# Kernel tuning notes

Measured on AMD Instinct MI355X. Metric: run time of the kernel, lower is better.

The kernel has to match this reference:

```python
import jax, jax.numpy as jnp
import numpy as np

B, T, D, H = 2, 2048, 1024, 16
HD = D // H


def sinusoidal_rel_pe(seq_len, d_model, dtype=jnp.float32):
    # Relative positions T-1 .. 0 (reversed), standard sin/cos interleave.
    pos = jnp.arange(seq_len - 1, -1, -1, dtype=jnp.float32)[:, None]  # [T,1]
    div = jnp.exp(-jnp.log(jnp.float32(10000.0)) * jnp.arange(0, d_model, 2, dtype=jnp.float32) / d_model)
    pe = jnp.zeros((seq_len, d_model), dtype=jnp.float32)
    pe = pe.at[:, 0::2].set(jnp.sin(pos * div))
    pe = pe.at[:, 1::2].set(jnp.cos(pos * div))
    return pe.astype(dtype)


def relative_to_absolute(x):
    # x: [B,H,T,L] with L == T. Music-Transformer skew trick.
    b, h, t1, l = x.shape
    x = jnp.pad(x, ((0, 0), (0, 0), (0, 0), (1, 0)))          # pad left of last dim
    x = x.reshape(b, h, -1)
    x = jnp.pad(x, ((0, 0), (0, 0), (l - t1, 0)))
    x = x.reshape(b, h, 1 + t1, l)
    return x[:, :, 1:]


def setup_inputs() -> dict:
    key = jax.random.key(0)
    k1, k2, k3 = jax.random.split(key, 3)
    x = jax.random.normal(k1, (B, T, D), dtype=jnp.float32)
    # causal mask: True where attention is disallowed (j > i)
    mask = jnp.triu(jnp.ones((T, T), dtype=bool), k=1)[None, None]
    mask = jnp.broadcast_to(mask, (B, 1, T, T))
    Wqkv = jax.random.normal(k2, (D, 3 * D), dtype=jnp.float32) * 0.02
    Wout = jax.random.normal(k3, (D, D), dtype=jnp.float32) * 0.02
    bout = jnp.zeros((D,), dtype=jnp.float32)
    return {"x": x, "mask": mask, "Wqkv": Wqkv, "Wout": Wout, "bout": bout}


def reference(x, mask, Wqkv, Wout, bout):
    b, t, d = x.shape
    scale = jnp.sqrt(jnp.float32(HD)).astype(x.dtype)
    qkv = x @ Wqkv                                  # [B,T,3D]
    q, k, v = jnp.split(qkv, 3, axis=-1)
    E = sinusoidal_rel_pe(t, d, x.dtype)            # [T,D], constant rel bias
    q = q.reshape(b, t, H, HD).transpose(0, 2, 1, 3)   # [B,H,T,hd]
    k = k.reshape(b, t, H, HD).transpose(0, 2, 1, 3)
    v = v.reshape(b, t, H, HD).transpose(0, 2, 1, 3)
    Eh = E.reshape(t, H, HD).transpose(1, 0, 2)        # [H,T,hd]
    att_k = jnp.einsum('bhqd,bhkd->bhqk', q, k)
    att_e = relative_to_absolute(jnp.einsum('bhqd,hkd->bhqk', q, Eh))
    score = (att_k + att_e) / scale
    score = jnp.where(mask, -jnp.inf, score)
    score = jax.nn.softmax(score, axis=-1)          # dropout is identity (eval)
    ctx = jnp.einsum('bhqk,bhkd->bhqd', score, v)
    ctx = ctx.transpose(0, 2, 1, 3).reshape(b, t, d)
    out = ctx @ Wout + bout
    return (out, score)
```

## Files before the change

kernel.cpp:

```cpp
#include <hip/hip_runtime.h>

typedef __bf16 bf16x8 __attribute__((ext_vector_type(8)));
typedef float f32x4 __attribute__((ext_vector_type(4)));

#define B_ 2
#define T_ 2048
#define D_ 1024
#define H_ 16

__device__ __forceinline__ ushort f2bf(float f) {
  union { float f; unsigned u; } v; v.f = f;
  unsigned u = v.u;
  return (ushort)((u + 0x7FFFu + ((u >> 16) & 1u)) >> 16);
}

__device__ __forceinline__ void g2l16(const void* g, void* l) {
  __builtin_amdgcn_global_load_lds(
      (const __attribute__((address_space(1))) unsigned int*)g,
      (__attribute__((address_space(3))) unsigned int*)l, 16, 0, 0);
}

__global__ __launch_bounds__(256) void cvt_kernel(const float* __restrict__ in,
                                                  ushort* __restrict__ out) {
  int i = (blockIdx.x * 256 + threadIdx.x) * 4;
  float4 v = *(const float4*)(in + i);
  ushort4 o;
  o.x = f2bf(v.x); o.y = f2bf(v.y); o.z = f2bf(v.z); o.w = f2bf(v.w);
  *(ushort4*)(out + i) = o;
}

__global__ void transpose_cvt(const float* __restrict__ in, ushort* __restrict__ out,
                              int R, int C) {
  __shared__ float tile[32][33];
  int bx = blockIdx.x * 32, by = blockIdx.y * 32;
  int tx = threadIdx.x, ty = threadIdx.y;
  for (int i = 0; i < 32; i += 8)
    tile[ty + i][tx] = in[(size_t)(by + ty + i) * C + (bx + tx)];
  __syncthreads();
  for (int i = 0; i < 32; i += 8)
    out[(size_t)(bx + ty + i) * R + (by + tx)] = f2bf(tile[tx][ty + i]);
}

__global__ __launch_bounds__(256) void gemm_bf16(
    const ushort* __restrict__ A, const ushort* __restrict__ BT,
    float* __restrict__ C, const float* __restrict__ bias,
    int M, int N, int K) {
  __shared__ alignas(16) ushort As[2][4096];
  __shared__ alignas(16) ushort Bs[2][4096];
  int tid = threadIdx.x;
  int wave = tid >> 6, lane = tid & 63;
  int l16 = lane & 15, lhi = lane >> 4;
  int m0 = blockIdx.y * 128, n0 = blockIdx.x * 128;
  int wr = (wave >> 1) * 64, wc = (wave & 1) * 64;
  int srow = lane >> 2, sch = lane & 3;

  f32x4 acc[4][4] = {};

  auto stage = [&](int kk, int buf) {
    for (int i = 0; i < 2; ++i) {
      int rg = i * 4 + wave;
      const ushort* ga = A + (size_t)(m0 + rg * 16 + srow) * K + kk + sch * 8;
      const ushort* gb = BT + (size_t)(n0 + rg * 16 + srow) * K + kk + sch * 8;
      g2l16(ga, &As[buf][rg * 512]);
      g2l16(gb, &Bs[buf][rg * 512]);
    }
  };

  stage(0, 0);
  int buf = 0;
  for (int kk = 0; kk < K; kk += 32) {
    __syncthreads();
    if (kk + 32 < K) stage(kk + 32, buf ^ 1);
    const ushort* Asb = As[buf];
    const ushort* Bsb = Bs[buf];
    bf16x8 af[4], bfr[4];
    for (int f = 0; f < 4; ++f)
      af[f] = *(const bf16x8*)(Asb + (wr + f * 16 + l16) * 32 + lhi * 8);
    for (int f = 0; f < 4; ++f)
      bfr[f] = *(const bf16x8*)(Bsb + (wc + f * 16 + l16) * 32 + lhi * 8);
    for (int fm = 0; fm < 4; ++fm)
      for (int fn = 0; fn < 4; ++fn)
        acc[fm][fn] = __builtin_amdgcn_mfma_f32_16x16x32_bf16(af[fm], bfr[fn], acc[fm][fn], 0, 0, 0);
    buf ^= 1;
  }
  for (int fm = 0; fm < 4; ++fm)
    for (int fn = 0; fn < 4; ++fn)
      for (int r = 0; r < 4; ++r) {
        int row = m0 + wr + fm * 16 + lhi * 4 + r;
        int col = n0 + wc + fn * 16 + l16;
        float v = acc[fm][fn][r];
        if (bias) v += bias[col];
        C[(size_t)row * N + col] = v;
      }
}

__global__ __launch_bounds__(256) void augment_kernel(
    const float* __restrict__ qkv,
    ushort* __restrict__ Qaug, ushort* __restrict__ Kaug, ushort* __restrict__ Vb) {
  int row = blockIdx.x;
  int b = row >> 11;
  int t = row & 2047;
  int tid = threadIdx.x;
  const float* src = qkv + (size_t)row * 3072;
  for (int i = 0; i < 4; ++i) {
    int idx = tid + i * 256;
    int h = idx >> 6, d = idx & 63;
    size_t obase = ((size_t)(b * H_ + h) * T_ + t);
    float q = src[idx];
    float k = src[1024 + idx];
    float v = src[2048 + idx];
    Qaug[obase * 128 + d] = f2bf(q * 0.125f);
    Kaug[obase * 128 + d] = f2bf(k);
    Vb[obase * 64 + d] = f2bf(v);
  }
  for (int i = 0; i < 2; ++i) {
    int idx = tid + i * 256;
    int h = idx >> 5, mm = idx & 31;
    int gdim = h * 64 + 2 * mm;
    float w = __expf(-9.2103403719761836f * (float)gdim * (1.0f / 1024.0f));
    float ang = w * (float)t;
    float si, co;
    __sincosf(ang, &si, &co);
    float qs = src[h * 64 + 2 * mm], qc = src[h * 64 + 2 * mm + 1];
    size_t obase = ((size_t)(b * H_ + h) * T_ + t);
    Qaug[obase * 128 + 64 + 2 * mm]     = f2bf((qs * si + qc * co) * 0.125f);
    Qaug[obase * 128 + 64 + 2 * mm + 1] = f2bf((qc * si - qs * co) * 0.125f);
    Kaug[obase * 128 + 64 + 2 * mm]     = f2bf(co);
    Kaug[obase * 128 + 64 + 2 * mm + 1] = f2bf(si);
  }
}

__global__ __launch_bounds__(256) void transpose_v(const ushort* __restrict__ Vb,
                                                   ushort* __restrict__ Vt) {
  __shared__ ushort tile[64][72];
  int bh = blockIdx.y, t0 = blockIdx.x * 64;
  int tid = threadIdx.x;
  for (int i = 0; i < 2; ++i) {
    int e = tid + i * 256;
    int row = e >> 3, ch = e & 7;
    *(int4*)(&tile[row][ch * 8]) =
        *(const int4*)(Vb + ((size_t)bh * T_ + t0 + row) * 64 + ch * 8);
  }
  __syncthreads();
  for (int i = 0; i < 2; ++i) {
    int e = tid + i * 256;
    int d = e >> 3, ch = e & 7;
    union { int4 v; ushort u[8]; } pk;
    for (int u = 0; u < 8; ++u) pk.u[u] = tile[ch * 8 + u][d];
    *(int4*)(Vt + ((size_t)bh * 64 + d) * T_ + t0 + ch * 8) = pk.v;
  }
}

__global__ __launch_bounds__(256) void attn_kernel(
    const ushort* __restrict__ Qaug,
    const ushort* __restrict__ Kaug,
    const ushort* __restrict__ Vt,
    float* __restrict__ score,
    ushort* __restrict__ ctxb) {
  int flat = blockIdx.y * 32 + blockIdx.x;
  int wg = (flat & 7) * 128 + (flat >> 3);
  int bh = wg >> 5;
  int qt = 31 - (wg & 31);
  int tid = threadIdx.x;
  int wave = tid >> 6, lane = tid & 63;
  int l16 = lane & 15, lhi = lane >> 4;
  int qb = wave * 16;
  int e7 = l16 & 7;

  __shared__ alignas(16) ushort Ks[2][8192];
  __shared__ alignas(16) ushort Vs[2][4096];
  __shared__ alignas(16) ushort Ps[4096];

  const ushort* Kbase = Kaug + (size_t)bh * T_ * 128;
  const ushort* Vbase = Vt + (size_t)bh * 64 * T_;

  auto stageK = [&](int kt, int buf) {
    for (int i = 0; i < 4; ++i) {
      int rg = i * 4 + wave;
      int key = rg * 4 + (lane >> 4);
      const ushort* g = Kbase + ((size_t)(kt * 64 + key)) * 128 + (((lane & 15) ^ (key & 7)) << 3);
      g2l16(g, &Ks[buf][rg * 512]);
    }
  };
  auto stageV = [&](int kt, int buf) {
    for (int i = 0; i < 2; ++i) {
      int rg = i * 4 + wave;
      int dim = rg * 8 + (lane >> 3);
      const ushort* g = Vbase + (size_t)dim * T_ + kt * 64 + (((lane & 7) ^ (dim & 7)) << 3);
      g2l16(g, &Vs[buf][rg * 512]);
    }
  };

  bf16x8 qf[4];
  {
    const ushort* Qg = Qaug + ((size_t)bh * T_ + qt * 64 + qb + l16) * 128;
    for (int ks = 0; ks < 4; ++ks)
      qf[ks] = *(const bf16x8*)(Qg + ks * 32 + lhi * 8);
  }

  stageK(0, 0);
  asm volatile("s_waitcnt vmcnt(0)" ::: "memory");
  __builtin_amdgcn_s_barrier();
  float plsum[4] = {0.f, 0.f, 0.f, 0.f};
  for (int kt = 0; kt <= qt; ++kt) {
    int buf = kt & 1;
    if (kt < qt) stageK(kt + 1, buf ^ 1);
    __builtin_amdgcn_sched_barrier(0);
    const ushort* Kb = Ks[buf];
    f32x4 s[4] = {};
    for (int ks = 0; ks < 4; ++ks)
      for (int fn = 0; fn < 4; ++fn) {
        bf16x8 bfr = *(const bf16x8*)(Kb + (fn * 16 + l16) * 128 + ((((ks << 2) | lhi) ^ e7) << 3));
        s[fn] = __builtin_amdgcn_mfma_f32_16x16x32_bf16(qf[ks], bfr, s[fn], 0, 0, 0);
      }
    if (kt == qt) {
      for (int fn = 0; fn < 4; ++fn)
        for (int r = 0; r < 4; ++r)
          if (fn * 16 + l16 > qb + lhi * 4 + r) s[fn][r] = -1e30f;
    }
    for (int r = 0; r < 4; ++r)
      plsum[r] += __expf(s[0][r]) + __expf(s[1][r]) + __expf(s[2][r]) + __expf(s[3][r]);
    if (kt < qt) {
      asm volatile("s_waitcnt vmcnt(0)" ::: "memory");
      __builtin_amdgcn_s_barrier();
    }
  }
  float invl[4];
  for (int r = 0; r < 4; ++r) {
    float v = plsum[r];
    for (int dd = 1; dd < 16; dd <<= 1) v += __shfl_xor(v, dd);
    invl[r] = 1.f / v;
  }

  __builtin_amdgcn_s_barrier();
  stageK(0, 0);
  stageV(0, 0);
  asm volatile("s_waitcnt vmcnt(0)" ::: "memory");
  __builtin_amdgcn_s_barrier();
  f32x4 cacc[4] = {};
  float* srow = score + ((size_t)bh * T_ + (size_t)qt * 64) * T_;

  for (int kt = 0; kt <= qt; ++kt) {
    int buf = kt & 1;
    if (kt < qt) { stageK(kt + 1, buf ^ 1); stageV(kt + 1, buf ^ 1); }
    __builtin_amdgcn_sched_barrier(0);
    const ushort* Kb = Ks[buf];
    f32x4 s[4] = {};
    for (int ks = 0; ks < 4; ++ks)
      for (int fn = 0; fn < 4; ++fn) {
        bf16x8 bfr = *(const bf16x8*)(Kb + (fn * 16 + l16) * 128 + ((((ks << 2) | lhi) ^ e7) << 3));
        s[fn] = __builtin_amdgcn_mfma_f32_16x16x32_bf16(qf[ks], bfr, s[fn], 0, 0, 0);
      }
    if (kt == qt) {
      for (int fn = 0; fn < 4; ++fn)
        for (int r = 0; r < 4; ++r)
          if (fn * 16 + l16 > qb + lhi * 4 + r) s[fn][r] = -1e30f;
    }
    for (int fn = 0; fn < 4; ++fn)
      for (int r = 0; r < 4; ++r) {
        int row_loc = qb + lhi * 4 + r;
        float p = __expf(s[fn][r]) * invl[r];
        srow[(size_t)row_loc * T_ + kt * 64 + fn * 16 + l16] = p;
        Ps[row_loc * 64 + (((fn * 2 + (l16 >> 3)) ^ (row_loc & 7)) << 3) + e7] = f2bf(p);
      }
    asm volatile("s_waitcnt lgkmcnt(0)" ::: "memory");
    __builtin_amdgcn_sched_barrier(0);
    const ushort* Vb2 = Vs[buf];
    for (int ks = 0; ks < 2; ++ks) {
      bf16x8 pa = *(const bf16x8*)(Ps + (qb + l16) * 64 + ((((ks << 2) | lhi) ^ e7) << 3));
      for (int fn = 0; fn < 4; ++fn) {
        bf16x8 vb = *(const bf16x8*)(Vb2 + (fn * 16 + l16) * 64 + ((((ks << 2) | lhi) ^ e7) << 3));
        cacc[fn] = __builtin_amdgcn_mfma_f32_16x16x32_bf16(pa, vb, cacc[fn], 0, 0, 0);
      }
    }
    if (kt < qt) {
      asm volatile("s_waitcnt vmcnt(16)" ::: "memory");
      __builtin_amdgcn_s_barrier();
    }
  }

  {
    int row = tid >> 2, c16 = (tid & 3) * 16;
    f32x4 z = {0.f, 0.f, 0.f, 0.f};
    for (int kt = qt + 1; kt < 32; ++kt) {
      f32x4* dst = (f32x4*)(srow + (size_t)row * T_ + kt * 64 + c16);
      for (int u = 0; u < 4; ++u) dst[u] = z;
    }
  }

  int b = bh >> 4, h = bh & 15;
  for (int fn = 0; fn < 4; ++fn)
    for (int r = 0; r < 4; ++r) {
      int t = qt * 64 + qb + lhi * 4 + r;
      int col = h * 64 + fn * 16 + l16;
      ctxb[((size_t)(b * T_ + t)) * 1024 + col] = f2bf(cacc[fn][r]);
    }
}

extern "C" void kernel_launch(void* const* d_in, const int* in_sizes, int n_in,
                              void* d_out, int out_size, void* d_ws, size_t ws_size,
                              hipStream_t stream) {
  const float* x    = (const float*)d_in[0];
  const float* Wqkv = (const float*)d_in[2];
  const float* Wout = (const float*)d_in[3];
  const float* bout = (const float*)d_in[4];

  char* ws = (char*)d_ws;
  ushort* xb    = (ushort*)(ws + 0);
  ushort* wqkvT = (ushort*)(ws + 8388608);
  ushort* woutT = (ushort*)(ws + 14680064);
  float*  qkv   = (float*) (ws + 16777216);
  ushort* Qaug  = (ushort*)(ws + 67108864);
  ushort* Kaug  = (ushort*)(ws + 83886080);
  ushort* Vb    = (ushort*)(ws + 100663296);
  ushort* ctxb  = (ushort*)(ws + 109051904);
  ushort* Vt    = (ushort*)(ws + 16777216);

  float* out   = (float*)d_out;
  float* score = out + (size_t)4194304;

  cvt_kernel<<<4096, 256, 0, stream>>>(x, xb);
  dim3 tb(32, 8);
  transpose_cvt<<<dim3(3072 / 32, 1024 / 32), tb, 0, stream>>>(Wqkv, wqkvT, 1024, 3072);
  transpose_cvt<<<dim3(1024 / 32, 1024 / 32), tb, 0, stream>>>(Wout, woutT, 1024, 1024);
  gemm_bf16<<<dim3(24, 32), 256, 0, stream>>>(xb, wqkvT, qkv, nullptr, 4096, 3072, 1024);
  augment_kernel<<<4096, 256, 0, stream>>>(qkv, Qaug, Kaug, Vb);
  transpose_v<<<dim3(32, 32), 256, 0, stream>>>(Vb, Vt);
  attn_kernel<<<dim3(32, 32), 256, 0, stream>>>(Qaug, Kaug, Vt, score, ctxb);
  gemm_bf16<<<dim3(8, 32), 256, 0, stream>>>(ctxb, woutT, out, bout, 4096, 1024, 1024);
}
```

Measured before the change: 316.3 us.

## Split attention into separate softmax-denominator and score/context kernels

The two-pass attention kernel is split in two. A lighter denom_kernel computes the row sums of exp and writes inverse denominators to workspace, using only the K buffers in shared memory and launch bounds that allow higher occupancy. A second kernel reads these values and does the score output and the P·V pass. The aim is to let the first pass run with less LDS and more waves per CU, at the cost of an extra launch and recomputing the Q fragment loads.

Result: no change. 316.6 us (+0.1%).

```diff
diff --git a/kernel.cpp b/kernel.cpp
--- a/kernel.cpp
+++ b/kernel.cpp
@@ -151,12 +151,10 @@
   }
 }
 
-__global__ __launch_bounds__(256) void attn_kernel(
+__global__ __launch_bounds__(256, 4) void denom_kernel(
     const ushort* __restrict__ Qaug,
     const ushort* __restrict__ Kaug,
-    const ushort* __restrict__ Vt,
-    float* __restrict__ score,
-    ushort* __restrict__ ctxb) {
+    float* __restrict__ invlb) {
   int flat = blockIdx.y * 32 + blockIdx.x;
   int wg = (flat & 7) * 128 + (flat >> 3);
   int bh = wg >> 5;
@@ -168,11 +166,8 @@
   int e7 = l16 & 7;
 
   __shared__ alignas(16) ushort Ks[2][8192];
-  __shared__ alignas(16) ushort Vs[2][4096];
-  __shared__ alignas(16) ushort Ps[4096];
 
   const ushort* Kbase = Kaug + (size_t)bh * T_ * 128;
-  const ushort* Vbase = Vt + (size_t)bh * 64 * T_;
 
   auto stageK = [&](int kt, int buf) {
     for (int i = 0; i < 4; ++i) {
@@ -180,14 +175,6 @@
       int key = rg * 4 + (lane >> 4);
       const ushort* g = Kbase + ((size_t)(kt * 64 + key)) * 128 + (((lane & 15) ^ (key & 7)) << 3);
       g2l16(g, &Ks[buf][rg * 512]);
-    }
-  };
-  auto stageV = [&](int kt, int buf) {
-    for (int i = 0; i < 2; ++i) {
-      int rg = i * 4 + wave;
-      int dim = rg * 8 + (lane >> 3);
-      const ushort* g = Vbase + (size_t)dim * T_ + kt * 64 + (((lane & 7) ^ (dim & 7)) << 3);
-      g2l16(g, &Vs[buf][rg * 512]);
     }
   };
 
@@ -225,14 +212,64 @@
       __builtin_amdgcn_s_barrier();
     }
   }
-  float invl[4];
   for (int r = 0; r < 4; ++r) {
     float v = plsum[r];
     for (int dd = 1; dd < 16; dd <<= 1) v += __shfl_xor(v, dd);
-    invl[r] = 1.f / v;
-  }
-
-  __builtin_amdgcn_s_barrier();
+    if (l16 == 0)
+      invlb[(size_t)bh * T_ + qt * 64 + qb + lhi * 4 + r] = 1.f / v;
+  }
+}
+
+__global__ __launch_bounds__(256) void attn2_kernel(
+    const ushort* __restrict__ Qaug,
+    const ushort* __restrict__ Kaug,
+    const ushort* __restrict__ Vt,
+    const float* __restrict__ invlb,
+    float* __restrict__ score,
+    ushort* __restrict__ ctxb) {
+  int flat = blockIdx.y * 32 + blockIdx.x;
+  int wg = (flat & 7) * 128 + (flat >> 3);
+  int bh = wg >> 5;
+  int qt = 31 - (wg & 31);
+  int tid = threadIdx.x;
+  int wave = tid >> 6, lane = tid & 63;
+  int l16 = lane & 15, lhi = lane >> 4;
+  int qb = wave * 16;
+  int e7 = l16 & 7;
+
+  __shared__ alignas(16) ushort Ks[2][8192];
+  __shared__ alignas(16) ushort Vs[2][4096];
+  __shared__ alignas(16) ushort Ps[4096];
+
+  const ushort* Kbase = Kaug + (size_t)bh * T_ * 128;
+  const ushort* Vbase = Vt + (size_t)bh * 64 * T_;
+
+  auto stageK = [&](int kt, int buf) {
+    for (int i = 0; i < 4; ++i) {
+      int rg = i * 4 + wave;
+      int key = rg * 4 + (lane >> 4);
+      const ushort* g = Kbase + ((size_t)(kt * 64 + key)) * 128 + (((lane & 15) ^ (key & 7)) << 3);
+      g2l16(g, &Ks[buf][rg * 512]);
+    }
+  };
+  auto stageV = [&](int kt, int buf) {
+    for (int i = 0; i < 2; ++i) {
+      int rg = i * 4 + wave;
+      int dim = rg * 8 + (lane >> 3);
+      const ushort* g = Vbase + (size_t)dim * T_ + kt * 64 + (((lane & 7) ^ (dim & 7)) << 3);
+      g2l16(g, &Vs[buf][rg * 512]);
+    }
+  };
+
+  bf16x8 qf[4];
+  {
+    const ushort* Qg = Qaug + ((size_t)bh * T_ + qt * 64 + qb + l16) * 128;
+    for (int ks = 0; ks < 4; ++ks)
+      qf[ks] = *(const bf16x8*)(Qg + ks * 32 + lhi * 8);
+  }
+  float4 iv = *(const float4*)(invlb + (size_t)bh * T_ + qt * 64 + qb + lhi * 4);
+  float invl[4] = {iv.x, iv.y, iv.z, iv.w};
+
   stageK(0, 0);
   stageV(0, 0);
   asm volatile("s_waitcnt vmcnt(0)" ::: "memory");
@@ -315,6 +352,7 @@
   ushort* Vb    = (ushort*)(ws + 100663296);
   ushort* ctxb  = (ushort*)(ws + 109051904);
   ushort* Vt    = (ushort*)(ws + 16777216);
+  float*  invlb = (float*) (ws + 25165824);
 
   float* out   = (float*)d_out;
   float* score = out + (size_t)4194304;
@@ -326,6 +364,7 @@
   gemm_bf16<<<dim3(24, 32), 256, 0, stream>>>(xb, wqkvT, qkv, nullptr, 4096, 3072, 1024);
   augment_kernel<<<4096, 256, 0, stream>>>(qkv, Qaug, Kaug, Vb);
   transpose_v<<<dim3(32, 32), 256, 0, stream>>>(Vb, Vt);
-  attn_kernel<<<dim3(32, 32), 256, 0, stream>>>(Qaug, Kaug, Vt, score, ctxb);
+  denom_kernel<<<dim3(32, 32), 256, 0, stream>>>(Qaug, Kaug, invlb);
+  attn2_kernel<<<dim3(32, 32), 256, 0, stream>>>(Qaug, Kaug, Vt, invlb, score, ctxb);
   gemm_bf16<<<dim3(8, 32), 256, 0, stream>>>(ctxb, woutT, out, bout, 4096, 1024, 1024);
 }
```

## Drop two-pass softmax: store unnormalized bf16 probs, normalize in separate kernel

Applied to the files above, without the earlier changes.

The attention kernel no longer runs a first pass over K to compute row sums. It now computes exp scores once, accumulates the row sum alongside the PV product, and writes unnormalized bf16 probabilities plus per-row inverse sums to workspace. The context is scaled by the inverse sum at the end. A new scale kernel reads the bf16 buffer, multiplies by the inverse sum and writes the fp32 score matrix, zero-filling the masked tail. This removes the duplicate QK^T pass at the cost of an extra bf16 round trip through memory and an added launch. Score values now go through bf16 rounding before output, which lowers their precision.

Measured after the change: 383.0 us. 1.21x slower.

```diff
diff --git a/kernel.cpp b/kernel.cpp
--- a/kernel.cpp
+++ b/kernel.cpp
@@ -12,6 +12,10 @@
   union { float f; unsigned u; } v; v.f = f;
   unsigned u = v.u;
   return (ushort)((u + 0x7FFFu + ((u >> 16) & 1u)) >> 16);
+}
+__device__ __forceinline__ float b2f(ushort u) {
+  union { unsigned u; float f; } v; v.u = ((unsigned)u) << 16;
+  return v.f;
 }
 
 __device__ __forceinline__ void g2l16(const void* g, void* l) {
@@ -151,11 +155,12 @@
   }
 }
 
-__global__ __launch_bounds__(256) void attn_kernel(
+__global__ __launch_bounds__(256) void attn_fused(
     const ushort* __restrict__ Qaug,
     const ushort* __restrict__ Kaug,
     const ushort* __restrict__ Vt,
-    float* __restrict__ score,
+    ushort* __restrict__ Pb,
+    float* __restrict__ invlb,
     ushort* __restrict__ ctxb) {
   int flat = blockIdx.y * 32 + blockIdx.x;
   int wg = (flat & 7) * 128 + (flat >> 3);
@@ -199,46 +204,11 @@
   }
 
   stageK(0, 0);
-  asm volatile("s_waitcnt vmcnt(0)" ::: "memory");
-  __builtin_amdgcn_s_barrier();
-  float plsum[4] = {0.f, 0.f, 0.f, 0.f};
-  for (int kt = 0; kt <= qt; ++kt) {
-    int buf = kt & 1;
-    if (kt < qt) stageK(kt + 1, buf ^ 1);
-    __builtin_amdgcn_sched_barrier(0);
-    const ushort* Kb = Ks[buf];
-    f32x4 s[4] = {};
-    for (int ks = 0; ks < 4; ++ks)
-      for (int fn = 0; fn < 4; ++fn) {
-        bf16x8 bfr = *(const bf16x8*)(Kb + (fn * 16 + l16) * 128 + ((((ks << 2) | lhi) ^ e7) << 3));
-        s[fn] = __builtin_amdgcn_mfma_f32_16x16x32_bf16(qf[ks], bfr, s[fn], 0, 0, 0);
-      }
-    if (kt == qt) {
-      for (int fn = 0; fn < 4; ++fn)
-        for (int r = 0; r < 4; ++r)
-          if (fn * 16 + l16 > qb + lhi * 4 + r) s[fn][r] = -1e30f;
-    }
-    for (int r = 0; r < 4; ++r)
-      plsum[r] += __expf(s[0][r]) + __expf(s[1][r]) + __expf(s[2][r]) + __expf(s[3][r]);
-    if (kt < qt) {
-      asm volatile("s_waitcnt vmcnt(0)" ::: "memory");
-      __builtin_amdgcn_s_barrier();
-    }
-  }
-  float invl[4];
-  for (int r = 0; r < 4; ++r) {
-    float v = plsum[r];
-    for (int dd = 1; dd < 16; dd <<= 1) v += __shfl_xor(v, dd);
-    invl[r] = 1.f / v;
-  }
-
-  __builtin_amdgcn_s_barrier();
-  stageK(0, 0);
   stageV(0, 0);
   asm volatile("s_waitcnt vmcnt(0)" ::: "memory");
   __builtin_amdgcn_s_barrier();
   f32x4 cacc[4] = {};
-  float* srow = score + ((size_t)bh * T_ + (size_t)qt * 64) * T_;
+  float plsum[4] = {0.f, 0.f, 0.f, 0.f};
 
   for (int kt = 0; kt <= qt; ++kt) {
     int buf = kt & 1;
@@ -259,8 +229,8 @@
     for (int fn = 0; fn < 4; ++fn)
       for (int r = 0; r < 4; ++r) {
         int row_loc = qb + lhi * 4 + r;
-        float p = __expf(s[fn][r]) * invl[r];
-        srow[(size_t)row_loc * T_ + kt * 64 + fn * 16 + l16] = p;
+        float p = __expf(s[fn][r]);
+        plsum[r] += p;
         Ps[row_loc * 64 + (((fn * 2 + (l16 >> 3)) ^ (row_loc & 7)) << 3) + e7] = f2bf(p);
       }
     asm volatile("s_waitcnt lgkmcnt(0)" ::: "memory");
@@ -273,19 +243,25 @@
         cacc[fn] = __builtin_amdgcn_mfma_f32_16x16x32_bf16(pa, vb, cacc[fn], 0, 0, 0);
       }
     }
+    for (int pass = 0; pass < 2; ++pass) {
+      int row_loc = qb + pass * 8 + (lane >> 3);
+      int j = lane & 7;
+      int4 u = *(const int4*)(Ps + row_loc * 64 + ((j ^ (row_loc & 7)) << 3));
+      *(int4*)(Pb + ((size_t)bh * T_ + qt * 64 + row_loc) * T_ + kt * 64 + j * 8) = u;
+    }
     if (kt < qt) {
-      asm volatile("s_waitcnt vmcnt(16)" ::: "memory");
+      asm volatile("s_waitcnt vmcnt(2)" ::: "memory");
       __builtin_amdgcn_s_barrier();
     }
   }
 
-  {
-    int row = tid >> 2, c16 = (tid & 3) * 16;
-    f32x4 z = {0.f, 0.f, 0.f, 0.f};
-    for (int kt = qt + 1; kt < 32; ++kt) {
-      f32x4* dst = (f32x4*)(srow + (size_t)row * T_ + kt * 64 + c16);
-      for (int u = 0; u < 4; ++u) dst[u] = z;
-    }
+  float invl[4];
+  for (int r = 0; r < 4; ++r) {
+    float v = plsum[r];
+    for (int dd = 1; dd < 16; dd <<= 1) v += __shfl_xor(v, dd);
+    invl[r] = 1.f / v;
+    if (l16 == 0)
+      invlb[(size_t)bh * T_ + qt * 64 + qb + lhi * 4 + r] = invl[r];
   }
 
   int b = bh >> 4, h = bh & 15;
@@ -293,8 +269,36 @@
     for (int r = 0; r < 4; ++r) {
       int t = qt * 64 + qb + lhi * 4 + r;
       int col = h * 64 + fn * 16 + l16;
-      ctxb[((size_t)(b * T_ + t)) * 1024 + col] = f2bf(cacc[fn][r]);
-    }
+      ctxb[((size_t)(b * T_ + t)) * 1024 + col] = f2bf(cacc[fn][r] * invl[r]);
+    }
+}
+
+__global__ __launch_bounds__(256) void scale_kernel(
+    const ushort* __restrict__ Pb, const float* __restrict__ invlb,
+    float* __restrict__ score) {
+  int wave = threadIdx.x >> 6, lane = threadIdx.x & 63;
+  int row0 = blockIdx.x * 16 + wave * 4;
+  for (int rr = 0; rr < 4; ++rr) {
+    int row = row0 + rr;
+    int t = row & 2047;
+    int L = ((t >> 6) + 1) << 6;
+    float inv = invlb[row];
+    const ushort* src = Pb + (size_t)row * 2048;
+    float* dst = score + (size_t)row * 2048;
+    for (int c = lane * 8; c < 2048; c += 512) {
+      f32x4 lo = {0.f, 0.f, 0.f, 0.f}, hi = {0.f, 0.f, 0.f, 0.f};
+      if (c < L) {
+        int4 u = *(const int4*)(src + c);
+        const ushort* us = (const ushort*)&u;
+        lo[0] = b2f(us[0]) * inv; lo[1] = b2f(us[1]) * inv;
+        lo[2] = b2f(us[2]) * inv; lo[3] = b2f(us[3]) * inv;
+        hi[0] = b2f(us[4]) * inv; hi[1] = b2f(us[5]) * inv;
+        hi[2] = b2f(us[6]) * inv; hi[3] = b2f(us[7]) * inv;
+      }
+      *(f32x4*)(dst + c) = lo;
+      *(f32x4*)(dst + c + 4) = hi;
+    }
+  }
 }
 
 extern "C" void kernel_launch(void* const* d_in, const int* in_sizes, int n_in,
@@ -315,6 +319,8 @@
   ushort* Vb    = (ushort*)(ws + 100663296);
   ushort* ctxb  = (ushort*)(ws + 109051904);
   ushort* Vt    = (ushort*)(ws + 16777216);
+  float*  invlb = (float*) (ws + 25165824);
+  ushort* Pb    = (ushort*)(ws + 134217728);
 
   float* out   = (float*)d_out;
   float* score = out + (size_t)4194304;
@@ -326,6 +332,7 @@
   gemm_bf16<<<dim3(24, 32), 256, 0, stream>>>(xb, wqkvT, qkv, nullptr, 4096, 3072, 1024);
   augment_kernel<<<4096, 256, 0, stream>>>(qkv, Qaug, Kaug, Vb);
   transpose_v<<<dim3(32, 32), 256, 0, stream>>>(Vb, Vt);
-  attn_kernel<<<dim3(32, 32), 256, 0, stream>>>(Qaug, Kaug, Vt, score, ctxb);
+  attn_fused<<<dim3(32, 32), 256, 0, stream>>>(Qaug, Kaug, Vt, Pb, invlb, ctxb);
+  scale_kernel<<<4096, 256, 0, stream>>>(Pb, invlb, score);
   gemm_bf16<<<dim3(8, 32), 256, 0, stream>>>(ctxb, woutT, out, bout, 4096, 1024, 1024);
 }
```
